# Kernel tuning notes

Hardware: AMD Instinct MI355X
Metric: run time of the kernel (lower is better)

## Reference

```python
import jax, jax.numpy as jnp
import numpy as np

B, Q, K, H, V = 16, 128, 512, 256, 256


def setup_inputs() -> dict:
    key = jax.random.key(0)
    ks = jax.random.split(key, 7)
    return {
        "queries": jax.random.normal(ks[0], (B, Q, H), dtype=jnp.float32),
        "keys": jax.random.normal(ks[1], (B, K, H), dtype=jnp.float32),
        "values": jax.random.normal(ks[2], (B, K, V), dtype=jnp.float32),
        "Wq": jax.random.normal(ks[3], (H, H), dtype=jnp.float32) / np.sqrt(H),
        "Wk": jax.random.normal(ks[4], (H, H), dtype=jnp.float32) / np.sqrt(H),
        "Wv": jax.random.normal(ks[5], (H,), dtype=jnp.float32) / np.sqrt(H),
        "valid_lens": jax.random.randint(ks[6], (B,), 1, K + 1, dtype=jnp.int32),
    }


def reference(queries, keys, values, Wq, Wk, Wv, valid_lens):
    # Projections (no bias, matching nn.Linear(..., bias=False))
    q = jnp.einsum("bqd,hd->bqh", queries, Wq)  # W_q: weight is [out,in] in torch; symmetric here
    k = jnp.einsum("bkd,hd->bkh", keys, Wk)
    # Broadcast add -> tanh -> project to scalar score: [B, Q, K]
    features = jnp.tanh(q[:, :, None, :] + k[:, None, :, :])  # [B,Q,K,H]
    scores = jnp.einsum("bqkh,h->bqk", features, Wv)
    # masked_softmax: positions >= valid_len get -1e6 before softmax
    mask = jnp.arange(K)[None, None, :] < valid_lens[:, None, None]  # [B,1,K]
    scores = jnp.where(mask, scores, -1e6)
    attn = jax.nn.softmax(scores, axis=-1)
    # dropout in eval mode = identity
    return jnp.einsum("bqk,bkv->bqv", attn, values)
```

## Files before the change

kernel.cpp:

```cpp
#include <hip/hip_runtime.h>

#define BQ   16
#define QLEN 128
#define KLEN 512
#define HD   256
#define VD   256

typedef __bf16 bf16x8 __attribute__((ext_vector_type(8)));
typedef float  f32x4  __attribute__((ext_vector_type(4)));

static __device__ __forceinline__ float fexp2(float x) {
#if __has_builtin(__builtin_amdgcn_exp2f)
    return __builtin_amdgcn_exp2f(x);
#else
    return exp2f(x);
#endif
}
static __device__ __forceinline__ float frcp(float x) {
#if __has_builtin(__builtin_amdgcn_rcpf)
    return __builtin_amdgcn_rcpf(x);
#else
    return 1.0f / x;
#endif
}

#define EXP_SCALE 2.8853900817779268f

__global__ __launch_bounds__(256) void mfma_proj(
    const float* __restrict__ queries, const float* __restrict__ keys,
    const float* __restrict__ Wq, const float* __restrict__ Wk,
    const int* __restrict__ vlen,
    float* __restrict__ Eq, float* __restrict__ Ekt)
{
    __shared__ __bf16 Ahi_s[64][40];
    __shared__ __bf16 Alo_s[64][40];
    __shared__ __bf16 Whi_s[64][40];
    __shared__ __bf16 Wlo_s[64][40];

    const int t    = threadIdx.x;
    const int ln   = t & 63;
    const int w    = t >> 6;
    const int p    = ln & 15;
    const int quad = ln >> 4;
    const int bx = blockIdx.x, by = blockIdx.y;
    const bool isq = by < 32;
    const int row0 = by * 64;
    const int col0 = bx * 64;

    if (!isq) {
        const int kr0 = row0 - 2048;
        if ((kr0 & 511) >= vlen[kr0 >> 9]) return;
    }

    const float* Ag = isq ? (queries + (size_t)row0 * HD)
                          : (keys + (size_t)(row0 - 2048) * HD);
    const float* Wg = isq ? Wq : Wk;

    const int ar = t >> 2, ac = (t & 3) * 8;

    float4 pa0, pa1, pw0, pw1;
    {
        const float* ap = Ag + ar * HD + ac;
        pa0 = *(const float4*)ap;
        pa1 = *(const float4*)(ap + 4);
        const float* wp = Wg + (size_t)(col0 + ar) * HD + ac;
        pw0 = *(const float4*)wp;
        pw1 = *(const float4*)(wp + 4);
    }

    f32x4 acc[4] = {};

    for (int s = 0; s < 8; ++s) {
        __syncthreads();
        {
            float fa[8] = {pa0.x, pa0.y, pa0.z, pa0.w, pa1.x, pa1.y, pa1.z, pa1.w};
            float fw[8] = {pw0.x, pw0.y, pw0.z, pw0.w, pw1.x, pw1.y, pw1.z, pw1.w};
            bf16x8 ha, la, hw, lw;
            #pragma unroll
            for (int j = 0; j < 8; ++j) {
                __bf16 av = (__bf16)fa[j];
                ha[j] = av;
                la[j] = (__bf16)(fa[j] - (float)av);
                __bf16 wv = (__bf16)fw[j];
                hw[j] = wv;
                lw[j] = (__bf16)(fw[j] - (float)wv);
            }
            *(bf16x8*)&Ahi_s[ar][ac] = ha;
            *(bf16x8*)&Alo_s[ar][ac] = la;
            *(bf16x8*)&Whi_s[ar][ac] = hw;
            *(bf16x8*)&Wlo_s[ar][ac] = lw;
        }
        __syncthreads();
        if (s < 7) {
            const int kc = (s + 1) * 32;
            const float* ap = Ag + ar * HD + kc + ac;
            pa0 = *(const float4*)ap;
            pa1 = *(const float4*)(ap + 4);
            const float* wp = Wg + (size_t)(col0 + ar) * HD + kc + ac;
            pw0 = *(const float4*)wp;
            pw1 = *(const float4*)(wp + 4);
        }
        bf16x8 bh = *(const bf16x8*)&Whi_s[w * 16 + p][quad * 8];
        bf16x8 bl = *(const bf16x8*)&Wlo_s[w * 16 + p][quad * 8];
        #pragma unroll
        for (int mi = 0; mi < 4; ++mi) {
            bf16x8 ah = *(const bf16x8*)&Ahi_s[mi * 16 + p][quad * 8];
            bf16x8 al = *(const bf16x8*)&Alo_s[mi * 16 + p][quad * 8];
            acc[mi] = __builtin_amdgcn_mfma_f32_16x16x32_bf16(ah, bh, acc[mi], 0, 0, 0);
            acc[mi] = __builtin_amdgcn_mfma_f32_16x16x32_bf16(ah, bl, acc[mi], 0, 0, 0);
            acc[mi] = __builtin_amdgcn_mfma_f32_16x16x32_bf16(al, bh, acc[mi], 0, 0, 0);
        }
    }

    #pragma unroll
    for (int mi = 0; mi < 4; ++mi) {
        const int H  = col0 + w * 16 + p;
        const int rl = mi * 16 + quad * 4;
        float e0 = fexp2(acc[mi][0] * EXP_SCALE);
        float e1 = fexp2(acc[mi][1] * EXP_SCALE);
        float e2 = fexp2(acc[mi][2] * EXP_SCALE);
        float e3 = fexp2(acc[mi][3] * EXP_SCALE);
        if (isq) {
            float* dst = Eq + (size_t)(row0 + rl) * HD + H;
            dst[0] = e0; dst[HD] = e1; dst[2 * HD] = e2; dst[3 * HD] = e3;
        } else {
            const int kr = row0 - 2048 + rl;
            const int b = kr >> 9, k0 = kr & 511;
            float4 st; st.x = e0; st.y = e1; st.z = e2; st.w = e3;
            *(float4*)(Ekt + ((size_t)b * HD + H) * KLEN + k0) = st;
        }
    }
}

__global__ __launch_bounds__(256) void proj_exp_gemm(
    const float* __restrict__ Qin, const float* __restrict__ Kin,
    const float* __restrict__ Wq, const float* __restrict__ Wk,
    float* __restrict__ Eq, float* __restrict__ Ekt)
{
    __shared__ union {
        struct { float a[2][16][68]; float w[2][16][68]; } s;
        float tb[64][65];
    } sh;

    const int t  = threadIdx.x;
    const int tx = t & 15, ty = t >> 4;
    const int bx = blockIdx.x, by = blockIdx.y;
    const bool isq = by < 32;
    const int row0 = isq ? by * 64 : (by - 32) * 64;
    const float* A = isq ? Qin : Kin;
    const float* W = isq ? Wq : Wk;
    const int lrow = t >> 2, ld0 = (t & 3) * 4;
    const float* Ab = A + (row0 + lrow) * HD;
    const float* Wb = W + (bx * 64 + lrow) * HD;

    float4 av = *(const float4*)(Ab + ld0);
    float4 wv = *(const float4*)(Wb + ld0);
    sh.s.a[0][ld0 + 0][lrow] = av.x; sh.s.a[0][ld0 + 1][lrow] = av.y;
    sh.s.a[0][ld0 + 2][lrow] = av.z; sh.s.a[0][ld0 + 3][lrow] = av.w;
    sh.s.w[0][ld0 + 0][lrow] = wv.x; sh.s.w[0][ld0 + 1][lrow] = wv.y;
    sh.s.w[0][ld0 + 2][lrow] = wv.z; sh.s.w[0][ld0 + 3][lrow] = wv.w;

    float acc[4][4] = {};
    int p = 0;
    for (int kc = 0; kc < HD; kc += 16) {
        if (kc + 16 < HD) {
            av = *(const float4*)(Ab + kc + 16 + ld0);
            wv = *(const float4*)(Wb + kc + 16 + ld0);
        }
        __syncthreads();
        if (kc + 16 < HD) {
            const int np = p ^ 1;
            sh.s.a[np][ld0 + 0][lrow] = av.x; sh.s.a[np][ld0 + 1][lrow] = av.y;
            sh.s.a[np][ld0 + 2][lrow] = av.z; sh.s.a[np][ld0 + 3][lrow] = av.w;
            sh.s.w[np][ld0 + 0][lrow] = wv.x; sh.s.w[np][ld0 + 1][lrow] = wv.y;
            sh.s.w[np][ld0 + 2][lrow] = wv.z; sh.s.w[np][ld0 + 3][lrow] = wv.w;
        }
        #pragma unroll
        for (int dd = 0; dd < 16; ++dd) {
            float4 a4 = *(const float4*)&sh.s.a[p][dd][ty * 4];
            float4 w4 = *(const float4*)&sh.s.w[p][dd][tx * 4];
            const float* af = (const float*)&a4;
            const float* wf = (const float*)&w4;
            #pragma unroll
            for (int i = 0; i < 4; ++i)
                #pragma unroll
                for (int j = 0; j < 4; ++j)
                    acc[i][j] = fmaf(af[i], wf[j], acc[i][j]);
        }
        p ^= 1;
    }

    float e[4][4];
    #pragma unroll
    for (int i = 0; i < 4; ++i)
        #pragma unroll
        for (int j = 0; j < 4; ++j)
            e[i][j] = fexp2(acc[i][j] * EXP_SCALE);

    if (isq) {
        float* Cb = Eq + (row0 + ty * 4) * HD + bx * 64 + tx * 4;
        #pragma unroll
        for (int i = 0; i < 4; ++i) {
            float4 st; st.x = e[i][0]; st.y = e[i][1]; st.z = e[i][2]; st.w = e[i][3];
            *(float4*)(Cb + i * HD) = st;
        }
    } else {
        __syncthreads();
        #pragma unroll
        for (int j = 0; j < 4; ++j) {
            float4 st; st.x = e[0][j]; st.y = e[1][j]; st.z = e[2][j]; st.w = e[3][j];
            *(float4*)&sh.tb[tx * 4 + j][ty * 4] = st;
        }
        __syncthreads();
        const int r = t >> 2, c0 = (t & 3) * 16;
        const int b = row0 >> 9, kbase = row0 & 511;
        float* dst = Ekt + ((size_t)b * HD + bx * 64 + r) * KLEN + kbase + c0;
        #pragma unroll
        for (int u = 0; u < 4; ++u) {
            float4 v = *(const float4*)&sh.tb[r][c0 + u * 4];
            *(float4*)(dst + u * 4) = v;
        }
    }
}

__global__ __launch_bounds__(512, 4) void fused_attn(
    const float* __restrict__ Eq, const float* __restrict__ Ekt,
    const float* __restrict__ values, const float* __restrict__ Wv,
    const int* __restrict__ vlen, float* __restrict__ out)
{
    __shared__ float eq_s[4][HD];
    __shared__ float wv_s[HD];
    __shared__ float sc[4][KLEN];
    __shared__ float ps[4][4][KLEN];
    __shared__ float wred[4];

    const int t    = threadIdx.x;
    const int b    = blockIdx.x >> 5;
    const int q0   = (blockIdx.x & 31) * 4;
    const int lane = t & 63;
    const int wid  = t >> 6;
    const int len  = vlen[b];

    {
        const int h = t & 255, rr = t >> 8;
        eq_s[rr][h]     = Eq[(b * QLEN + q0 + rr) * HD + h];
        eq_s[rr + 2][h] = Eq[(b * QLEN + q0 + rr + 2) * HD + h];
        if (t < HD) {
            float w = Wv[t];
            wv_s[t] = w;
            float ws = w;
            #pragma unroll
            for (int off = 32; off > 0; off >>= 1) ws += __shfl_xor(ws, off, 64);
            if (lane == 0) wred[wid] = ws;
        }
    }
    __syncthreads();
    const float wv_sum = wred[0] + wred[1] + wred[2] + wred[3];

    const int hs    = wid & 3, khalf = wid >> 2;
    if (khalf * 256 < len) {
        const int hbase = hs * 64;
        const int k4    = khalf * 256 + lane * 4;
        const float* ek = Ekt + ((size_t)b * HD + hbase) * KLEN + k4;
        float acc[4][4] = {};
        float4 n0 = *(const float4*)(ek + 0 * KLEN);
        float4 n1 = *(const float4*)(ek + 1 * KLEN);
        float4 n2 = *(const float4*)(ek + 2 * KLEN);
        float4 n3 = *(const float4*)(ek + 3 * KLEN);
        for (int hh = 0; hh < 64; hh += 4) {
            float4 e0 = n0, e1 = n1, e2 = n2, e3 = n3;
            if (hh + 4 < 64) {
                const float* nk = ek + (size_t)(hh + 4) * KLEN;
                n0 = *(const float4*)(nk + 0 * KLEN);
                n1 = *(const float4*)(nk + 1 * KLEN);
                n2 = *(const float4*)(nk + 2 * KLEN);
                n3 = *(const float4*)(nk + 3 * KLEN);
            }
            const float* E0 = (const float*)&e0;
            const float* E1 = (const float*)&e1;
            const float* E2 = (const float*)&e2;
            const float* E3 = (const float*)&e3;
            const float w0 = wv_s[hbase + hh + 0], w1 = wv_s[hbase + hh + 1];
            const float w2 = wv_s[hbase + hh + 2], w3 = wv_s[hbase + hh + 3];
            #pragma unroll
            for (int i = 0; i < 4; ++i) {
                const float a0 = eq_s[i][hbase + hh + 0], a1 = eq_s[i][hbase + hh + 1];
                const float a2 = eq_s[i][hbase + hh + 2], a3 = eq_s[i][hbase + hh + 3];
                #pragma unroll
                for (int j = 0; j < 4; ++j) {
                    float d0 = fmaf(a0, E0[j], 1.f);
                    float d1 = fmaf(a1, E1[j], 1.f);
                    float d2 = fmaf(a2, E2[j], 1.f);
                    float d3 = fmaf(a3, E3[j], 1.f);
                    float d01 = d0 * d1, d23 = d2 * d3;
                    float n01 = fmaf(w1, d0, w0 * d1);
                    float n23 = fmaf(w3, d2, w2 * d3);
                    float top = fmaf(n23, d01, n01 * d23);
                    acc[i][j] = fmaf(top, frcp(d01 * d23), acc[i][j]);
                }
            }
        }
        #pragma unroll
        for (int i = 0; i < 4; ++i) {
            float4 st; st.x = acc[i][0]; st.y = acc[i][1]; st.z = acc[i][2]; st.w = acc[i][3];
            *(float4*)&ps[hs][i][k4] = st;
        }
    }
    __syncthreads();

    if (wid < 4) {
        float s[8];
        float m = -3.0e38f;
        #pragma unroll
        for (int j = 0; j < 8; ++j) {
            int k = lane + j * 64;
            float raw = ps[0][wid][k] + ps[1][wid][k] + ps[2][wid][k] + ps[3][wid][k];
            float v = fmaf(-2.f, raw, wv_sum);
            v = (k < len) ? v : -1.0e6f;
            s[j] = v;
            m = fmaxf(m, v);
        }
        #pragma unroll
        for (int off = 32; off > 0; off >>= 1) m = fmaxf(m, __shfl_xor(m, off, 64));
        float sum = 0.f;
        #pragma unroll
        for (int j = 0; j < 8; ++j) {
            float ev = fexp2(1.4426950408889634f * (s[j] - m));
            s[j] = ev;
            sum += ev;
        }
        #pragma unroll
        for (int off = 32; off > 0; off >>= 1) sum += __shfl_xor(sum, off, 64);
        const float rs = frcp(sum);
        #pragma unroll
        for (int j = 0; j < 8; ++j) sc[wid][lane + j * 64] = s[j] * rs;
    }
    __syncthreads();

    float (*po)[4][VD] = (float (*)[4][VD])ps;
    const int c4 = lane * 4;
    if (wid * 64 < len) {
        const float* vb = values + (size_t)b * KLEN * VD + (size_t)(wid * 64) * VD + c4;
        float o[4][4] = {};
        for (int kk = 0; kk < 64; kk += 4) {
            const int k = wid * 64 + kk;
            float4 pr[4];
            pr[0] = *(const float4*)&sc[0][k];
            pr[1] = *(const float4*)&sc[1][k];
            pr[2] = *(const float4*)&sc[2][k];
            pr[3] = *(const float4*)&sc[3][k];
            #pragma unroll
            for (int j = 0; j < 4; ++j) {
                float4 v4 = *(const float4*)(vb + (size_t)(kk + j) * VD);
                #pragma unroll
                for (int r = 0; r < 4; ++r) {
                    float pj = ((const float*)&pr[r])[j];
                    o[r][0] = fmaf(pj, v4.x, o[r][0]);
                    o[r][1] = fmaf(pj, v4.y, o[r][1]);
                    o[r][2] = fmaf(pj, v4.z, o[r][2]);
                    o[r][3] = fmaf(pj, v4.w, o[r][3]);
                }
            }
        }
        #pragma unroll
        for (int r = 0; r < 4; ++r) {
            float4 st; st.x = o[r][0]; st.y = o[r][1]; st.z = o[r][2]; st.w = o[r][3];
            *(float4*)&po[wid][r][c4] = st;
        }
    } else {
        float4 z; z.x = z.y = z.z = z.w = 0.f;
        #pragma unroll
        for (int r = 0; r < 4; ++r) *(float4*)&po[wid][r][c4] = z;
    }
    __syncthreads();

    #pragma unroll
    for (int u = 0; u < 2; ++u) {
        int idx = t + u * 512;
        int r = idx >> 8, c = idx & 255;
        float s = 0.f;
        #pragma unroll
        for (int sl = 0; sl < 8; ++sl) s += po[sl][r][c];
        out[(b * QLEN + q0 + r) * VD + c] = s;
    }
}

extern "C" void kernel_launch(void* const* d_in, const int* in_sizes, int n_in,
                              void* d_out, int out_size, void* d_ws, size_t ws_size,
                              hipStream_t stream) {
    const float* queries = (const float*)d_in[0];
    const float* keys    = (const float*)d_in[1];
    const float* values  = (const float*)d_in[2];
    const float* Wq      = (const float*)d_in[3];
    const float* Wk      = (const float*)d_in[4];
    const float* Wv      = (const float*)d_in[5];
    const int*   vl      = (const int*)d_in[6];
    float* out = (float*)d_out;

    float* Eq  = (float*)d_ws;
    float* Ekt = Eq + 2048 * 256;

    if (ws_size >= 10485760) {
        mfma_proj<<<dim3(4, 160), 256, 0, stream>>>(queries, keys, Wq, Wk, vl, Eq, Ekt);
    } else {
        proj_exp_gemm<<<dim3(4, 160), 256, 0, stream>>>(queries, keys, Wq, Wk, Eq, Ekt);
    }
    fused_attn<<<dim3(512), 512, 0, stream>>>(Eq, Ekt, values, Wv, vl, out);
}
```

Before: 116.9 us.

## Reassign score and PV work per wave to shrink LDS and raise occupancy

The score phase now gives each wave 64 keys across the full hidden dimension with one key per lane. The partial-sum buffer and its cross-wave reduction are gone, and scores are written straight into the softmax buffer. The PV phase splits into four key quarters by two value halves, with a lane shuffle reduction, which halves the partial-output buffer. Launch bounds are raised to 8 blocks per CU. Scalar Ekt loads replace float4 loads and each lane does less work per loaded element, so LDS and register savings are traded against lower ILP and load width.

```diff
diff --git a/kernel.cpp b/kernel.cpp
--- a/kernel.cpp
+++ b/kernel.cpp
@@ -223,7 +223,7 @@
     }
 }
 
-__global__ __launch_bounds__(512, 4) void fused_attn(
+__global__ __launch_bounds__(512, 8) void fused_attn(
     const float* __restrict__ Eq, const float* __restrict__ Ekt,
     const float* __restrict__ values, const float* __restrict__ Wv,
     const int* __restrict__ vlen, float* __restrict__ out)
@@ -231,7 +231,7 @@
     __shared__ float eq_s[4][HD];
     __shared__ float wv_s[HD];
     __shared__ float sc[4][KLEN];
-    __shared__ float ps[4][4][KLEN];
+    __shared__ float po[4][4][VD];
     __shared__ float wred[4];
 
     const int t    = threadIdx.x;
@@ -257,54 +257,34 @@
     __syncthreads();
     const float wv_sum = wred[0] + wred[1] + wred[2] + wred[3];
 
-    const int hs    = wid & 3, khalf = wid >> 2;
-    if (khalf * 256 < len) {
-        const int hbase = hs * 64;
-        const int k4    = khalf * 256 + lane * 4;
-        const float* ek = Ekt + ((size_t)b * HD + hbase) * KLEN + k4;
-        float acc[4][4] = {};
-        float4 n0 = *(const float4*)(ek + 0 * KLEN);
-        float4 n1 = *(const float4*)(ek + 1 * KLEN);
-        float4 n2 = *(const float4*)(ek + 2 * KLEN);
-        float4 n3 = *(const float4*)(ek + 3 * KLEN);
-        for (int hh = 0; hh < 64; hh += 4) {
-            float4 e0 = n0, e1 = n1, e2 = n2, e3 = n3;
-            if (hh + 4 < 64) {
+    if (wid * 64 < len) {
+        const int k = wid * 64 + lane;
+        const float* ek = Ekt + (size_t)b * HD * KLEN + k;
+        float acc[4] = {};
+        float n0 = ek[0], n1 = ek[KLEN], n2 = ek[2 * KLEN], n3 = ek[3 * KLEN];
+        for (int hh = 0; hh < HD; hh += 4) {
+            float e0 = n0, e1 = n1, e2 = n2, e3 = n3;
+            if (hh + 4 < HD) {
                 const float* nk = ek + (size_t)(hh + 4) * KLEN;
-                n0 = *(const float4*)(nk + 0 * KLEN);
-                n1 = *(const float4*)(nk + 1 * KLEN);
-                n2 = *(const float4*)(nk + 2 * KLEN);
-                n3 = *(const float4*)(nk + 3 * KLEN);
+                n0 = nk[0]; n1 = nk[KLEN]; n2 = nk[2 * KLEN]; n3 = nk[3 * KLEN];
             }
-            const float* E0 = (const float*)&e0;
-            const float* E1 = (const float*)&e1;
-            const float* E2 = (const float*)&e2;
-            const float* E3 = (const float*)&e3;
-            const float w0 = wv_s[hbase + hh + 0], w1 = wv_s[hbase + hh + 1];
-            const float w2 = wv_s[hbase + hh + 2], w3 = wv_s[hbase + hh + 3];
+            float4 w4 = *(const float4*)&wv_s[hh];
             #pragma unroll
             for (int i = 0; i < 4; ++i) {
-                const float a0 = eq_s[i][hbase + hh + 0], a1 = eq_s[i][hbase + hh + 1];
-                const float a2 = eq_s[i][hbase + hh + 2], a3 = eq_s[i][hbase + hh + 3];
-                #pragma unroll
-                for (int j = 0; j < 4; ++j) {
-                    float d0 = fmaf(a0, E0[j], 1.f);
-                    float d1 = fmaf(a1, E1[j], 1.f);
-                    float d2 = fmaf(a2, E2[j], 1.f);
-                    float d3 = fmaf(a3, E3[j], 1.f);
-                    float d01 = d0 * d1, d23 = d2 * d3;
-                    float n01 = fmaf(w1, d0, w0 * d1);
-                    float n23 = fmaf(w3, d2, w2 * d3);
-                    float top = fmaf(n23, d01, n01 * d23);
-                    acc[i][j] = fmaf(top, frcp(d01 * d23), acc[i][j]);
-                }
+                float4 a4 = *(const float4*)&eq_s[i][hh];
+                float d0 = fmaf(a4.x, e0, 1.f);
+                float d1 = fmaf(a4.y, e1, 1.f);
+                float d2 = fmaf(a4.z, e2, 1.f);
+                float d3 = fmaf(a4.w, e3, 1.f);
+                float d01 = d0 * d1, d23 = d2 * d3;
+                float n01 = fmaf(w4.y, d0, w4.x * d1);
+                float n23 = fmaf(w4.w, d2, w4.z * d3);
+                float top = fmaf(n23, d01, n01 * d23);
+                acc[i] = fmaf(top, frcp(d01 * d23), acc[i]);
             }
         }
         #pragma unroll
-        for (int i = 0; i < 4; ++i) {
-            float4 st; st.x = acc[i][0]; st.y = acc[i][1]; st.z = acc[i][2]; st.w = acc[i][3];
-            *(float4*)&ps[hs][i][k4] = st;
-        }
+        for (int i = 0; i < 4; ++i) sc[i][k] = fmaf(-2.f, acc[i], wv_sum);
     }
     __syncthreads();
 
@@ -314,8 +294,7 @@
         #pragma unroll
         for (int j = 0; j < 8; ++j) {
             int k = lane + j * 64;
-            float raw = ps[0][wid][k] + ps[1][wid][k] + ps[2][wid][k] + ps[3][wid][k];
-            float v = fmaf(-2.f, raw, wv_sum);
+            float v = sc[wid][k];
             v = (k < len) ? v : -1.0e6f;
             s[j] = v;
             m = fmaxf(m, v);
@@ -337,40 +316,42 @@
     }
     __syncthreads();
 
-    float (*po)[4][VD] = (float (*)[4][VD])ps;
-    const int c4 = lane * 4;
-    if (wid * 64 < len) {
-        const float* vb = values + (size_t)b * KLEN * VD + (size_t)(wid * 64) * VD + c4;
+    const int kq = wid & 3, vh = wid >> 2;
+    const int kk = lane >> 5, vv = lane & 31;
+    const int v0 = vh * 128 + vv * 4;
+    if (kq * 128 < len) {
+        const float* vb = values + (size_t)b * KLEN * VD + (size_t)(kq * 128 + kk) * VD + v0;
         float o[4][4] = {};
-        for (int kk = 0; kk < 64; kk += 4) {
-            const int k = wid * 64 + kk;
-            float4 pr[4];
-            pr[0] = *(const float4*)&sc[0][k];
-            pr[1] = *(const float4*)&sc[1][k];
-            pr[2] = *(const float4*)&sc[2][k];
-            pr[3] = *(const float4*)&sc[3][k];
-            #pragma unroll
-            for (int j = 0; j < 4; ++j) {
-                float4 v4 = *(const float4*)(vb + (size_t)(kk + j) * VD);
-                #pragma unroll
-                for (int r = 0; r < 4; ++r) {
-                    float pj = ((const float*)&pr[r])[j];
-                    o[r][0] = fmaf(pj, v4.x, o[r][0]);
-                    o[r][1] = fmaf(pj, v4.y, o[r][1]);
-                    o[r][2] = fmaf(pj, v4.z, o[r][2]);
-                    o[r][3] = fmaf(pj, v4.w, o[r][3]);
-                }
+        for (int ks = 0; ks < 128; ks += 2) {
+            const int k = kq * 128 + ks + kk;
+            float4 v4 = *(const float4*)(vb + (size_t)ks * VD);
+            float p0 = sc[0][k], p1 = sc[1][k], p2 = sc[2][k], p3 = sc[3][k];
+            o[0][0] = fmaf(p0, v4.x, o[0][0]); o[0][1] = fmaf(p0, v4.y, o[0][1]);
+            o[0][2] = fmaf(p0, v4.z, o[0][2]); o[0][3] = fmaf(p0, v4.w, o[0][3]);
+            o[1][0] = fmaf(p1, v4.x, o[1][0]); o[1][1] = fmaf(p1, v4.y, o[1][1]);
+            o[1][2] = fmaf(p1, v4.z, o[1][2]); o[1][3] = fmaf(p1, v4.w, o[1][3]);
+            o[2][0] = fmaf(p2, v4.x, o[2][0]); o[2][1] = fmaf(p2, v4.y, o[2][1]);
+            o[2][2] = fmaf(p2, v4.z, o[2][2]); o[2][3] = fmaf(p2, v4.w, o[2][3]);
+            o[3][0] = fmaf(p3, v4.x, o[3][0]); o[3][1] = fmaf(p3, v4.y, o[3][1]);
+            o[3][2] = fmaf(p3, v4.z, o[3][2]); o[3][3] = fmaf(p3, v4.w, o[3][3]);
+        }
+        #pragma unroll
+        for (int r = 0; r < 4; ++r) {
+            #pragma unroll
+            for (int c = 0; c < 4; ++c) o[r][c] += __shfl_xor(o[r][c], 32, 64);
+        }
+        if (kk == 0) {
+            #pragma unroll
+            for (int r = 0; r < 4; ++r) {
+                float4 st; st.x = o[r][0]; st.y = o[r][1]; st.z = o[r][2]; st.w = o[r][3];
+                *(float4*)&po[kq][r][v0] = st;
             }
         }
-        #pragma unroll
-        for (int r = 0; r < 4; ++r) {
-            float4 st; st.x = o[r][0]; st.y = o[r][1]; st.z = o[r][2]; st.w = o[r][3];
-            *(float4*)&po[wid][r][c4] = st;
-        }
     } else {
+        const int zq = lane >> 4, zx = vh * 128 + (lane & 15) * 8;
         float4 z; z.x = z.y = z.z = z.w = 0.f;
-        #pragma unroll
-        for (int r = 0; r < 4; ++r) *(float4*)&po[wid][r][c4] = z;
+        *(float4*)&po[kq][zq][zx]     = z;
+        *(float4*)&po[kq][zq][zx + 4] = z;
     }
     __syncthreads();
 
@@ -378,10 +359,8 @@
     for (int u = 0; u < 2; ++u) {
         int idx = t + u * 512;
         int r = idx >> 8, c = idx & 255;
-        float s = 0.f;
-        #pragma unroll
-        for (int sl = 0; sl < 8; ++sl) s += po[sl][r][c];
-        out[(b * QLEN + q0 + r) * VD + c] = s;
+        out[(b * QLEN + q0 + r) * VD + c] =
+            po[0][r][c] + po[1][r][c] + po[2][r][c] + po[3][r][c];
     }
 }
 
```

After: 140.5 us. 20.2% more time.

## Rebalance score and PV work across all waves for short valid lengths

Applied to the files above, without the earlier changes.

When valid_len is at most 256, all eight waves now split the hidden dimension of the score computation into 32-wide slices over the first 256 keys, instead of half the waves going idle. The P·V stage is also restructured so each wave covers 128 value columns over a key quarter, with two key rows per iteration folded together by a lane shuffle. Only four partial output slices are reduced at the end. The score stage always runs the 256-key-wide tile regardless of len, and the P·V stage now loads values for masked keys where the old code skipped them. This trades some redundant work for even load balance across waves.

```diff
diff --git a/kernel.cpp b/kernel.cpp
--- a/kernel.cpp
+++ b/kernel.cpp
@@ -240,6 +240,7 @@
     const int lane = t & 63;
     const int wid  = t >> 6;
     const int len  = vlen[b];
+    const bool small = (len <= 256);
 
     {
         const int h = t & 255, rr = t >> 8;
@@ -257,19 +258,22 @@
     __syncthreads();
     const float wv_sum = wred[0] + wred[1] + wred[2] + wred[3];
 
-    const int hs    = wid & 3, khalf = wid >> 2;
-    if (khalf * 256 < len) {
-        const int hbase = hs * 64;
-        const int k4    = khalf * 256 + lane * 4;
-        const float* ek = Ekt + ((size_t)b * HD + hbase) * KLEN + k4;
-        float acc[4][4] = {};
+    {
+        const int hbase = small ? (wid * 32) : ((wid & 3) * 64);
+        const int hcnt  = small ? 32 : 64;
+        const int kload = small ? (lane * 4) : ((wid >> 2) * 256 + lane * 4);
+        const int col   = (wid >> 2) * 256 + lane * 4;
+        const float* ek = Ekt + ((size_t)b * HD + hbase) * KLEN + kload;
+        float acc[4] = {};
+        float accb[4] = {};
         float4 n0 = *(const float4*)(ek + 0 * KLEN);
         float4 n1 = *(const float4*)(ek + 1 * KLEN);
         float4 n2 = *(const float4*)(ek + 2 * KLEN);
         float4 n3 = *(const float4*)(ek + 3 * KLEN);
-        for (int hh = 0; hh < 64; hh += 4) {
+        float acc2[4][4] = {};
+        for (int hh = 0; hh < hcnt; hh += 4) {
             float4 e0 = n0, e1 = n1, e2 = n2, e3 = n3;
-            if (hh + 4 < 64) {
+            if (hh + 4 < hcnt) {
                 const float* nk = ek + (size_t)(hh + 4) * KLEN;
                 n0 = *(const float4*)(nk + 0 * KLEN);
                 n1 = *(const float4*)(nk + 1 * KLEN);
@@ -296,14 +300,15 @@
                     float n01 = fmaf(w1, d0, w0 * d1);
                     float n23 = fmaf(w3, d2, w2 * d3);
                     float top = fmaf(n23, d01, n01 * d23);
-                    acc[i][j] = fmaf(top, frcp(d01 * d23), acc[i][j]);
+                    acc2[i][j] = fmaf(top, frcp(d01 * d23), acc2[i][j]);
                 }
             }
         }
+        (void)acc; (void)accb;
         #pragma unroll
         for (int i = 0; i < 4; ++i) {
-            float4 st; st.x = acc[i][0]; st.y = acc[i][1]; st.z = acc[i][2]; st.w = acc[i][3];
-            *(float4*)&ps[hs][i][k4] = st;
+            float4 st; st.x = acc2[i][0]; st.y = acc2[i][1]; st.z = acc2[i][2]; st.w = acc2[i][3];
+            *(float4*)&ps[wid & 3][i][col] = st;
         }
     }
     __syncthreads();
@@ -311,14 +316,30 @@
     if (wid < 4) {
         float s[8];
         float m = -3.0e38f;
-        #pragma unroll
-        for (int j = 0; j < 8; ++j) {
-            int k = lane + j * 64;
-            float raw = ps[0][wid][k] + ps[1][wid][k] + ps[2][wid][k] + ps[3][wid][k];
-            float v = fmaf(-2.f, raw, wv_sum);
-            v = (k < len) ? v : -1.0e6f;
-            s[j] = v;
-            m = fmaxf(m, v);
+        if (small) {
+            #pragma unroll
+            for (int j = 0; j < 4; ++j) {
+                int k = lane + j * 64;
+                float raw = ps[0][wid][k] + ps[1][wid][k] + ps[2][wid][k] + ps[3][wid][k]
+                          + ps[0][wid][k + 256] + ps[1][wid][k + 256]
+                          + ps[2][wid][k + 256] + ps[3][wid][k + 256];
+                float v = fmaf(-2.f, raw, wv_sum);
+                v = (k < len) ? v : -1.0e6f;
+                s[j] = v;
+                m = fmaxf(m, v);
+            }
+            #pragma unroll
+            for (int j = 4; j < 8; ++j) s[j] = -1.0e6f;
+        } else {
+            #pragma unroll
+            for (int j = 0; j < 8; ++j) {
+                int k = lane + j * 64;
+                float raw = ps[0][wid][k] + ps[1][wid][k] + ps[2][wid][k] + ps[3][wid][k];
+                float v = fmaf(-2.f, raw, wv_sum);
+                v = (k < len) ? v : -1.0e6f;
+                s[j] = v;
+                m = fmaxf(m, v);
+            }
         }
         #pragma unroll
         for (int off = 32; off > 0; off >>= 1) m = fmaxf(m, __shfl_xor(m, off, 64));
@@ -332,45 +353,46 @@
         #pragma unroll
         for (int off = 32; off > 0; off >>= 1) sum += __shfl_xor(sum, off, 64);
         const float rs = frcp(sum);
-        #pragma unroll
-        for (int j = 0; j < 8; ++j) sc[wid][lane + j * 64] = s[j] * rs;
+        const int jmax = small ? 4 : 8;
+        for (int j = 0; j < jmax; ++j) sc[wid][lane + j * 64] = s[j] * rs;
     }
     __syncthreads();
 
     float (*po)[4][VD] = (float (*)[4][VD])ps;
-    const int c4 = lane * 4;
-    if (wid * 64 < len) {
-        const float* vb = values + (size_t)b * KLEN * VD + (size_t)(wid * 64) * VD + c4;
+    const int kq = wid & 3, vh = wid >> 2;
+    const int kk = lane >> 5, vv = lane & 31;
+    const int v0 = vh * 128 + vv * 4;
+    const int kbase = small ? kq * 64 : kq * 128;
+    const int kcnt  = small ? 64 : 128;
+    {
+        const float* vb = values + (size_t)b * KLEN * VD + (size_t)(kbase + kk) * VD + v0;
         float o[4][4] = {};
-        for (int kk = 0; kk < 64; kk += 4) {
-            const int k = wid * 64 + kk;
-            float4 pr[4];
-            pr[0] = *(const float4*)&sc[0][k];
-            pr[1] = *(const float4*)&sc[1][k];
-            pr[2] = *(const float4*)&sc[2][k];
-            pr[3] = *(const float4*)&sc[3][k];
-            #pragma unroll
-            for (int j = 0; j < 4; ++j) {
-                float4 v4 = *(const float4*)(vb + (size_t)(kk + j) * VD);
-                #pragma unroll
-                for (int r = 0; r < 4; ++r) {
-                    float pj = ((const float*)&pr[r])[j];
-                    o[r][0] = fmaf(pj, v4.x, o[r][0]);
-                    o[r][1] = fmaf(pj, v4.y, o[r][1]);
-                    o[r][2] = fmaf(pj, v4.z, o[r][2]);
-                    o[r][3] = fmaf(pj, v4.w, o[r][3]);
-                }
-            }
-        }
+        for (int ks = 0; ks < kcnt; ks += 2) {
+            const int k = kbase + ks + kk;
+            float4 v4 = *(const float4*)(vb + (size_t)ks * VD);
+            float p0 = sc[0][k], p1 = sc[1][k], p2 = sc[2][k], p3 = sc[3][k];
+            o[0][0] = fmaf(p0, v4.x, o[0][0]); o[0][1] = fmaf(p0, v4.y, o[0][1]);
+            o[0][2] = fmaf(p0, v4.z, o[0][2]); o[0][3] = fmaf(p0, v4.w, o[0][3]);
+            o[1][0] = fmaf(p1, v4.x, o[1][0]); o[1][1] = fmaf(p1, v4.y, o[1][1]);
+            o[1][2] = fmaf(p1, v4.z, o[1][2]); o[1][3] = fmaf(p1, v4.w, o[1][3]);
+            o[2][0] = fmaf(p2, v4.x, o[2][0]); o[2][1] = fmaf(p2, v4.y, o[2][1]);
+            o[2][2] = fmaf(p2, v4.z, o[2][2]); o[2][3] = fmaf(p2, v4.w, o[2][3]);
+            o[3][0] = fmaf(p3, v4.x, o[3][0]); o[3][1] = fmaf(p3, v4.y, o[3][1]);
+            o[3][2] = fmaf(p3, v4.z, o[3][2]); o[3][3] = fmaf(p3, v4.w, o[3][3]);
+        }
+        __syncthreads();
         #pragma unroll
         for (int r = 0; r < 4; ++r) {
-            float4 st; st.x = o[r][0]; st.y = o[r][1]; st.z = o[r][2]; st.w = o[r][3];
-            *(float4*)&po[wid][r][c4] = st;
-        }
-    } else {
-        float4 z; z.x = z.y = z.z = z.w = 0.f;
-        #pragma unroll
-        for (int r = 0; r < 4; ++r) *(float4*)&po[wid][r][c4] = z;
+            #pragma unroll
+            for (int c = 0; c < 4; ++c) o[r][c] += __shfl_xor(o[r][c], 32, 64);
+        }
+        if (kk == 0) {
+            #pragma unroll
+            for (int r = 0; r < 4; ++r) {
+                float4 st; st.x = o[r][0]; st.y = o[r][1]; st.z = o[r][2]; st.w = o[r][3];
+                *(float4*)&po[kq][r][v0] = st;
+            }
+        }
     }
     __syncthreads();
 
@@ -378,10 +400,8 @@
     for (int u = 0; u < 2; ++u) {
         int idx = t + u * 512;
         int r = idx >> 8, c = idx & 255;
-        float s = 0.f;
-        #pragma unroll
-        for (int sl = 0; sl < 8; ++sl) s += po[sl][r][c];
-        out[(b * QLEN + q0 + r) * VD + c] = s;
+        out[(b * QLEN + q0 + r) * VD + c] =
+            po[0][r][c] + po[1][r][c] + po[2][r][c] + po[3][r][c];
     }
 }
 
```

After: 132.2 us. 13.0% more time.
